# Performance work log

Hardware: AMD Instinct MI355X
Metric: run time of the kernel (lower is better)

Reference implementation:

```python
import jax, jax.numpy as jnp
import numpy as np
from jax import lax


def _b_mask(out_c, in_c, kh, kw):
    # MaskedConv2d mask_type='B' for a 1xK kernel: zero strictly right-of-center taps
    m = np.ones((out_c, in_c, kh, kw), dtype=np.float32)
    m[:, :, kh // 2:, kw // 2 + 1:] = 0
    m[:, :, kh // 2 + 1:, :] = 0
    return jnp.asarray(m)


def _conv(x, w, b):
    # NCHW 'same' conv, stride 1
    y = lax.conv_general_dilated(x, w, (1, 1), 'SAME',
                                 dimension_numbers=('NCHW', 'OIHW', 'NCHW'))
    return y + b[None, :, None, None]


def setup_inputs() -> dict:
    key = jax.random.key(0)
    ks = jax.random.split(key, 7)
    B, C_in, H, W = 32, 3, 64, 64
    HC = 128
    return {
        'x': jax.random.normal(ks[0], (B, C_in, H, W), jnp.float32),
        'W_is': jax.random.normal(ks[1], (4 * HC, C_in, 1, 3), jnp.float32) * 0.1,
        'b_is': jax.random.normal(ks[2], (4 * HC,), jnp.float32) * 0.1,
        'W_ss': jax.random.normal(ks[3], (4 * HC, HC, 1, 3), jnp.float32) * 0.1,
        'b_ss': jax.random.normal(ks[4], (4 * HC,), jnp.float32) * 0.1,
        'h0': jax.random.normal(ks[5], (1, HC, 1, W), jnp.float32) * 0.05,
        'c0': jax.random.normal(ks[6], (1, HC, 1, W), jnp.float32) * 0.05,
    }


def reference(x, W_is, b_is, W_ss, b_ss, h0, c0):
    B, _, H, W = x.shape
    HC = h0.shape[1]
    W_is_m = W_is * _b_mask(*W_is.shape)
    W_ss_m = W_ss * _b_mask(*W_ss.shape)

    # input-to-state projection for all rows at once: [B, 4*HC, H, W]
    x_proj = _conv(x, W_is_m, b_is)
    x_rows = jnp.moveaxis(x_proj, 2, 0)[:, :, :, None, :]  # [H, B, 4HC, 1, W]

    h_init = jnp.broadcast_to(h0, (B, HC, 1, W))
    c_init = jnp.broadcast_to(c0, (B, HC, 1, W))

    def step(carry, row_x):
        h_prev, c_prev = carry
        gates = jax.nn.sigmoid(row_x + _conv(h_prev, W_ss_m, b_ss))
        o, f, i, g = jnp.split(gates, 4, axis=1)
        c = f * c_prev + i * g
        h = o * jnp.tanh(c)
        return (h, c), h

    _, hs = lax.scan(step, (h_init, c_init), x_rows)  # hs: [H, B, HC, 1, W]
    hidden = jnp.moveaxis(hs[:, :, :, 0, :], 0, 2)  # [B, HC, H, W]
    return hidden
```

## Files before the change

kernel.cpp:

```cpp
#include <hip/hip_runtime.h>
#include <hip/hip_bf16.h>

typedef unsigned short u16;
typedef unsigned int u32;
typedef unsigned long long u64;
typedef short bf16x8 __attribute__((ext_vector_type(8)));
typedef float f32x4  __attribute__((ext_vector_type(4)));


__device__ __forceinline__ u16 f2b(float f) {
    return __builtin_bit_cast(u16, __float2bfloat16(f));
}
__device__ __forceinline__ float sigm(float x) {
    return __builtin_amdgcn_rcpf(1.0f + __expf(-x));
}
__device__ __forceinline__ float tanh_fast(float x) {
    return 1.0f - 2.0f * __builtin_amdgcn_rcpf(__expf(2.0f * x) + 1.0f);
}

#define LINE(kt, lane) (((kt) * 64 + (lane)) * 16)
#define BUFBYTES (9 * 64 * 16)

__global__ __launch_bounds__(512, 2) void rowlstm_mfma8(
    const float* __restrict__ x,   const float* __restrict__ Wis,
    const float* __restrict__ bis, const float* __restrict__ Wss,
    const float* __restrict__ bss, const float* __restrict__ h0,
    const float* __restrict__ c0,  float* __restrict__ out,
    char* halo)
{
    __shared__ __align__(16) char lds_buf[2 * BUFBYTES];
    __shared__ u16  lds_x[3 * 64 * 17];
    __shared__ float lds_bias[512];

    const int tid  = threadIdx.x;
    const int s    = blockIdx.x;
    const int b    = blockIdx.y;
    const int wid  = tid >> 6;
    const int lane = tid & 63;
    const int q    = lane >> 4;
    const int n    = lane & 15;
    const int wbase = s * 16;

    char* hs_my = halo + ((size_t)(b * 4 + s) * 64) * 256;
    char* hs_up = halo + ((size_t)(b * 4 + (s > 0 ? s - 1 : 0)) * 64) * 256;

    for (int i = tid; i < 1152; i += 512)
        *(uint4*)(lds_buf + i * 16) = make_uint4(0, 0, 0, 0);
    __syncthreads();

    lds_bias[tid] = bis[tid] + bss[tid];

    for (int i = tid; i < 3264; i += 512) {
        int cch = i / 1088, rem = i % 1088;
        int r = rem / 17, wl1 = rem % 17;
        int gw = wbase + wl1 - 1;
        lds_x[i] = (gw < 0) ? (u16)0
                 : f2b(x[(((size_t)b * 3 + cch) * 64 + r) * 64 + gw]);
    }

    bf16x8 afr[4][9];
    {
        #pragma unroll
        for (int g = 0; g < 4; ++g) {
            int oc = g * 128 + wid * 16 + n;
            #pragma unroll
            for (int kt = 0; kt < 8; ++kt) {
                bf16x8 a;
                #pragma unroll
                for (int jj = 0; jj < 4; ++jj) {
                    int ic = kt * 16 + q * 4 + jj;
                    float2 wp = *(const float2*)&Wss[(size_t)(oc * 128 + ic) * 3];
                    a[jj]     = (short)f2b(wp.y);
                    a[4 + jj] = (short)f2b(wp.x);
                }
                afr[g][kt] = a;
            }
            bf16x8 ax = {0, 0, 0, 0, 0, 0, 0, 0};
            if (q == 0) {
                #pragma unroll
                for (int cch = 0; cch < 3; ++cch) {
                    float2 wp = *(const float2*)&Wis[(size_t)(oc * 3 + cch) * 3];
                    ax[cch]     = (short)f2b(wp.y);
                    ax[4 + cch] = (short)f2b(wp.x);
                }
            }
            afr[g][8] = ax;
        }
    }

    float cst[4];
    {
        u16 hw[4];
        #pragma unroll
        for (int reg = 0; reg < 4; ++reg) {
            int hc = wid * 16 + q * 4 + reg;
            int wg = wbase + n;
            cst[reg] = c0[hc * 64 + wg];
            hw[reg] = f2b(h0[hc * 64 + wg]);
        }
        u64 d01 = (u64)((u32)hw[0] | ((u32)hw[1] << 16))
                | ((u64)((u32)hw[2] | ((u32)hw[3] << 16)) << 32);
        *(u64*)(lds_buf + LINE(wid, lane)) = d01;
        int wl = n + 1;
        if (wl < 16)
            *(u64*)(lds_buf + LINE(wid, q * 16 + wl) + 8) = d01;
    }
    if (s > 0 && tid < 32) {
        int ic0 = tid * 4;
        u64 v = (u64)((u32)f2b(h0[(ic0 + 0) * 64 + wbase - 1]) | ((u32)f2b(h0[(ic0 + 1) * 64 + wbase - 1]) << 16))
              | ((u64)((u32)f2b(h0[(ic0 + 2) * 64 + wbase - 1]) | ((u32)f2b(h0[(ic0 + 3) * 64 + wbase - 1]) << 16)) << 32);
        *(u64*)(lds_buf + LINE(tid >> 2, (tid & 3) * 16) + 8) = v;
    }
    if (tid < 16) {
        int nn = tid;
        u32 d0 = (u32)lds_x[0 * 1088 + 0 * 17 + nn + 1] | ((u32)lds_x[1 * 1088 + 0 * 17 + nn + 1] << 16);
        u32 d1 = (u32)lds_x[2 * 1088 + 0 * 17 + nn + 1];
        u32 d2 = (u32)lds_x[0 * 1088 + 0 * 17 + nn]     | ((u32)lds_x[1 * 1088 + 0 * 17 + nn] << 16);
        u32 d3 = (u32)lds_x[2 * 1088 + 0 * 17 + nn];
        *(uint4*)(lds_buf + LINE(8, nn)) = make_uint4(d0, d1, d2, d3);
    }
    __syncthreads();

    f32x4 bias_r[4];
    #pragma unroll
    for (int g = 0; g < 4; ++g) {
        int oc = g * 128 + wid * 16 + q * 4;
        bias_r[g][0] = lds_bias[oc + 0];
        bias_r[g][1] = lds_bias[oc + 1];
        bias_r[g][2] = lds_bias[oc + 2];
        bias_r[g][3] = lds_bias[oc + 3];
    }

    u64 hv = 0, hn = 0;
    const bool is_cons = (s > 0) && (tid < 32);
    if (is_cons)
        hv = __hip_atomic_load((const u64*)(hs_up + (size_t)tid * 8),
                               __ATOMIC_RELAXED, __HIP_MEMORY_SCOPE_AGENT);

    for (int r = 0; r < 64; ++r) {
        char* rbuf = lds_buf + (r & 1) * BUFBYTES;
        char* wbuf = lds_buf + ((r & 1) ^ 1) * BUFBYTES;

        if (is_cons && r < 62)
            hn = __hip_atomic_load((const u64*)(hs_up + (size_t)(r + 1) * 256 + tid * 8),
                                   __ATOMIC_RELAXED, __HIP_MEMORY_SCOPE_AGENT);

        if (r < 63 && tid >= 64 && tid < 80) {
            int nn = tid - 64, r1 = r + 1;
            u32 d0 = (u32)lds_x[0 * 1088 + r1 * 17 + nn + 1] | ((u32)lds_x[1 * 1088 + r1 * 17 + nn + 1] << 16);
            u32 d1 = (u32)lds_x[2 * 1088 + r1 * 17 + nn + 1];
            u32 d2 = (u32)lds_x[0 * 1088 + r1 * 17 + nn]     | ((u32)lds_x[1 * 1088 + r1 * 17 + nn] << 16);
            u32 d3 = (u32)lds_x[2 * 1088 + r1 * 17 + nn];
            *(uint4*)(wbuf + LINE(8, nn)) = make_uint4(d0, d1, d2, d3);
        }

        f32x4 acc[4];
        acc[0] = bias_r[0]; acc[1] = bias_r[1];
        acc[2] = bias_r[2]; acc[3] = bias_r[3];
        #pragma unroll
        for (int kt = 0; kt < 9; ++kt) {
            bf16x8 bv = *(const bf16x8*)(rbuf + LINE(kt, lane));
            acc[0] = __builtin_amdgcn_mfma_f32_16x16x32_bf16(afr[0][kt], bv, acc[0], 0, 0, 0);
            acc[1] = __builtin_amdgcn_mfma_f32_16x16x32_bf16(afr[1][kt], bv, acc[1], 0, 0, 0);
            acc[2] = __builtin_amdgcn_mfma_f32_16x16x32_bf16(afr[2][kt], bv, acc[2], 0, 0, 0);
            acc[3] = __builtin_amdgcn_mfma_f32_16x16x32_bf16(afr[3][kt], bv, acc[3], 0, 0, 0);
        }

        float hval[4]; u16 hw[4];
        #pragma unroll
        for (int reg = 0; reg < 4; ++reg) {
            float o  = sigm(acc[0][reg]);
            float f  = sigm(acc[1][reg]);
            float ii = sigm(acc[2][reg]);
            float gg = sigm(acc[3][reg]);
            float cn = f * cst[reg] + ii * gg;
            cst[reg] = cn;
            float h = o * tanh_fast(cn);
            hval[reg] = h;
            hw[reg] = f2b(h);
        }

        u64 d01 = (u64)((u32)hw[0] | ((u32)hw[1] << 16))
                | ((u64)((u32)hw[2] | ((u32)hw[3] << 16)) << 32);
        *(u64*)(wbuf + LINE(wid, lane)) = d01;
        int wl = n + 1;
        if (wl < 16) {
            *(u64*)(wbuf + LINE(wid, q * 16 + wl) + 8) = d01;
        } else if (s < 3 && r < 63) {
            __hip_atomic_store((u64*)(hs_my + (size_t)r * 256 + (wid * 4 + q) * 8),
                               ~d01, __ATOMIC_RELAXED, __HIP_MEMORY_SCOPE_AGENT);
        }

        #pragma unroll
        for (int reg = 0; reg < 4; ++reg) {
            int hc = wid * 16 + q * 4 + reg;
            out[(((size_t)(b * 128 + hc)) * 64 + r) * 64 + wbase + n] = hval[reg];
        }

        if (is_cons && r < 63) {
            while (hv == 0) {
                __builtin_amdgcn_s_sleep(1);
                hv = __hip_atomic_load((const u64*)(hs_up + (size_t)r * 256 + tid * 8),
                                       __ATOMIC_RELAXED, __HIP_MEMORY_SCOPE_AGENT);
            }
            *(u64*)(wbuf + LINE(tid >> 2, (tid & 3) * 16) + 8) = ~hv;
            hv = hn;
        }

        __builtin_amdgcn_sched_barrier(0);
        asm volatile("s_waitcnt lgkmcnt(0)\n\ts_barrier" ::: "memory");
        __builtin_amdgcn_sched_barrier(0);
    }
}

extern "C" void kernel_launch(void* const* d_in, const int* in_sizes, int n_in,
                              void* d_out, int out_size, void* d_ws, size_t ws_size,
                              hipStream_t stream)
{
    const float* x   = (const float*)d_in[0];
    const float* Wis = (const float*)d_in[1];
    const float* bis = (const float*)d_in[2];
    const float* Wss = (const float*)d_in[3];
    const float* bss = (const float*)d_in[4];
    const float* h0  = (const float*)d_in[5];
    const float* c0  = (const float*)d_in[6];
    float* out = (float*)d_out;

    hipMemsetAsync(d_ws, 0, (size_t)32 * 4 * 64 * 256, stream);
    rowlstm_mfma8<<<dim3(4, 32), 512, 0, stream>>>(
        x, Wis, bis, Wss, bss, h0, c0, out, (char*)d_ws);
}
```

Baseline: 205.5 us.

## Replace per-row workgroup barrier with per-wave LDS progress flags

```diff
diff --git a/kernel.cpp b/kernel.cpp
--- a/kernel.cpp
+++ b/kernel.cpp
@@ -20,8 +20,9 @@
 
 #define LINE(kt, lane) (((kt) * 64 + (lane)) * 16)
 #define BUFBYTES (9 * 64 * 16)
-
-__global__ __launch_bounds__(512, 2) void rowlstm_mfma8(
+#define SPIN_CAP (1 << 16)
+
+__global__ __launch_bounds__(512, 2) void rowlstm_mfma10(
     const float* __restrict__ x,   const float* __restrict__ Wis,
     const float* __restrict__ bis, const float* __restrict__ Wss,
     const float* __restrict__ bss, const float* __restrict__ h0,
@@ -31,6 +32,7 @@
     __shared__ __align__(16) char lds_buf[2 * BUFBYTES];
     __shared__ u16  lds_x[3 * 64 * 17];
     __shared__ float lds_bias[512];
+    __shared__ u32  wdone[8];
 
     const int tid  = threadIdx.x;
     const int s    = blockIdx.x;
@@ -46,6 +48,7 @@
 
     for (int i = tid; i < 1152; i += 512)
         *(uint4*)(lds_buf + i * 16) = make_uint4(0, 0, 0, 0);
+    if (tid < 8) wdone[tid] = 0;
     __syncthreads();
 
     lds_bias[tid] = bis[tid] + bss[tid];
@@ -132,9 +135,9 @@
     }
 
     u64 hv = 0, hn = 0;
-    const bool is_cons = (s > 0) && (tid < 32);
+    const bool is_cons = (s > 0) && (lane < 4);
     if (is_cons)
-        hv = __hip_atomic_load((const u64*)(hs_up + (size_t)tid * 8),
+        hv = __hip_atomic_load((const u64*)(hs_up + (size_t)(wid * 4 + lane) * 8),
                                __ATOMIC_RELAXED, __HIP_MEMORY_SCOPE_AGENT);
 
     for (int r = 0; r < 64; ++r) {
@@ -142,24 +145,32 @@
         char* wbuf = lds_buf + ((r & 1) ^ 1) * BUFBYTES;
 
         if (is_cons && r < 62)
-            hn = __hip_atomic_load((const u64*)(hs_up + (size_t)(r + 1) * 256 + tid * 8),
+            hn = __hip_atomic_load((const u64*)(hs_up + (size_t)(r + 1) * 256 + (wid * 4 + lane) * 8),
                                    __ATOMIC_RELAXED, __HIP_MEMORY_SCOPE_AGENT);
 
-        if (r < 63 && tid >= 64 && tid < 80) {
-            int nn = tid - 64, r1 = r + 1;
-            u32 d0 = (u32)lds_x[0 * 1088 + r1 * 17 + nn + 1] | ((u32)lds_x[1 * 1088 + r1 * 17 + nn + 1] << 16);
-            u32 d1 = (u32)lds_x[2 * 1088 + r1 * 17 + nn + 1];
-            u32 d2 = (u32)lds_x[0 * 1088 + r1 * 17 + nn]     | ((u32)lds_x[1 * 1088 + r1 * 17 + nn] << 16);
-            u32 d3 = (u32)lds_x[2 * 1088 + r1 * 17 + nn];
-            *(uint4*)(wbuf + LINE(8, nn)) = make_uint4(d0, d1, d2, d3);
-        }
+        u32 f[8];
+        #pragma unroll
+        for (int j = 0; j < 8; ++j)
+            f[j] = __hip_atomic_load(&wdone[j], __ATOMIC_RELAXED,
+                                     __HIP_MEMORY_SCOPE_WORKGROUP);
 
         f32x4 acc[4];
         acc[0] = bias_r[0]; acc[1] = bias_r[1];
         acc[2] = bias_r[2]; acc[3] = bias_r[3];
         #pragma unroll
         for (int kt = 0; kt < 9; ++kt) {
-            bf16x8 bv = *(const bf16x8*)(rbuf + LINE(kt, lane));
+            const int g = (kt < 8) ? kt : 1;
+            if (f[g] < (u32)r) {
+                int guard = 0;
+                do {
+                    __builtin_amdgcn_s_sleep(1);
+                    f[g] = __hip_atomic_load(&wdone[g], __ATOMIC_RELAXED,
+                                             __HIP_MEMORY_SCOPE_WORKGROUP);
+                } while (f[g] < (u32)r && ++guard < SPIN_CAP);
+            }
+            int off = LINE(kt, lane);
+            asm volatile("" : "+v"(off) : "v"(f[g]));
+            bf16x8 bv = *(const bf16x8*)(rbuf + off);
             acc[0] = __builtin_amdgcn_mfma_f32_16x16x32_bf16(afr[0][kt], bv, acc[0], 0, 0, 0);
             acc[1] = __builtin_amdgcn_mfma_f32_16x16x32_bf16(afr[1][kt], bv, acc[1], 0, 0, 0);
             acc[2] = __builtin_amdgcn_mfma_f32_16x16x32_bf16(afr[2][kt], bv, acc[2], 0, 0, 0);
@@ -170,10 +181,10 @@
         #pragma unroll
         for (int reg = 0; reg < 4; ++reg) {
             float o  = sigm(acc[0][reg]);
-            float f  = sigm(acc[1][reg]);
+            float f_ = sigm(acc[1][reg]);
             float ii = sigm(acc[2][reg]);
             float gg = sigm(acc[3][reg]);
-            float cn = f * cst[reg] + ii * gg;
+            float cn = f_ * cst[reg] + ii * gg;
             cst[reg] = cn;
             float h = o * tanh_fast(cn);
             hval[reg] = h;
@@ -191,24 +202,40 @@
                                ~d01, __ATOMIC_RELAXED, __HIP_MEMORY_SCOPE_AGENT);
         }
 
+        if (r < 63 && tid >= 64 && tid < 80) {
+            int nn = tid - 64, r1 = r + 1;
+            u32 d0 = (u32)lds_x[0 * 1088 + r1 * 17 + nn + 1] | ((u32)lds_x[1 * 1088 + r1 * 17 + nn + 1] << 16);
+            u32 d1 = (u32)lds_x[2 * 1088 + r1 * 17 + nn + 1];
+            u32 d2 = (u32)lds_x[0 * 1088 + r1 * 17 + nn]     | ((u32)lds_x[1 * 1088 + r1 * 17 + nn] << 16);
+            u32 d3 = (u32)lds_x[2 * 1088 + r1 * 17 + nn];
+            *(uint4*)(wbuf + LINE(8, nn)) = make_uint4(d0, d1, d2, d3);
+        }
+
+        if (is_cons && r < 63) {
+            if (hv == 0) {
+                int guard = 0;
+                do {
+                    __builtin_amdgcn_s_sleep(1);
+                    hv = __hip_atomic_load((const u64*)(hs_up + (size_t)r * 256 + (wid * 4 + lane) * 8),
+                                           __ATOMIC_RELAXED, __HIP_MEMORY_SCOPE_AGENT);
+                } while (hv == 0 && ++guard < SPIN_CAP);
+            }
+            *(u64*)(wbuf + LINE(wid, lane * 16) + 8) = ~hv;
+            hv = hn;
+        }
+
         #pragma unroll
         for (int reg = 0; reg < 4; ++reg) {
             int hc = wid * 16 + q * 4 + reg;
             out[(((size_t)(b * 128 + hc)) * 64 + r) * 64 + wbase + n] = hval[reg];
         }
 
-        if (is_cons && r < 63) {
-            while (hv == 0) {
-                __builtin_amdgcn_s_sleep(1);
-                hv = __hip_atomic_load((const u64*)(hs_up + (size_t)r * 256 + tid * 8),
-                                       __ATOMIC_RELAXED, __HIP_MEMORY_SCOPE_AGENT);
-            }
-            *(u64*)(wbuf + LINE(tid >> 2, (tid & 3) * 16) + 8) = ~hv;
-            hv = hn;
-        }
-
         __builtin_amdgcn_sched_barrier(0);
-        asm volatile("s_waitcnt lgkmcnt(0)\n\ts_barrier" ::: "memory");
+        asm volatile("s_waitcnt lgkmcnt(0)" ::: "memory");
+        __builtin_amdgcn_sched_barrier(0);
+        if (lane == 0)
+            __hip_atomic_store(&wdone[wid], (u32)(r + 1), __ATOMIC_RELAXED,
+                               __HIP_MEMORY_SCOPE_WORKGROUP);
         __builtin_amdgcn_sched_barrier(0);
     }
 }
@@ -227,6 +254,6 @@
     float* out = (float*)d_out;
 
     hipMemsetAsync(d_ws, 0, (size_t)32 * 4 * 64 * 256, stream);
-    rowlstm_mfma8<<<dim3(4, 32), 512, 0, stream>>>(
+    rowlstm_mfma10<<<dim3(4, 32), 512, 0, stream>>>(
         x, Wis, bis, Wss, bss, h0, c0, out, (char*)d_ws);
 }
```

New measurement: 230.9 us. 12.4% more time.
